# Performance work log

Measured on AMD Instinct MI355X. Metric: run time of the kernel, lower is better.

Reference implementation:

```python
import jax, jax.numpy as jnp
import numpy as np

B, L, D, O = 4, 256, 512, 128

def setup_inputs() -> dict:
    key = jax.random.key(0)
    k1, k2, k3, k4, k5, k6 = jax.random.split(key, 6)
    return {
        "x1": jax.random.normal(k1, (B, L, D), jnp.float32),
        "x2": jax.random.normal(k2, (B, L, D), jnp.float32),
        "bw": jax.random.uniform(k3, (2,), jnp.float32),
        "W_bil": jax.random.normal(k4, (O, D + 1, D + 1), jnp.float32) * 0.02,
        "W_lin": jax.random.normal(k5, (2 * D, O), jnp.float32) * 0.02,
        "b_lin": jax.random.normal(k6, (O,), jnp.float32) * 0.02,
    }

def reference(x1, x2, bw, W_bil, W_lin, b_lin):
    bwn = jax.nn.softmax(bw)
    d1 = x1.shape[-1]
    # Bilinear with bias_x/bias_y: append ones column to x1 and x2.
    ones1 = jnp.ones((*x1.shape[:2], 1), x1.dtype)
    ones2 = jnp.ones((*x2.shape[:2], 1), x2.dtype)
    x1b = jnp.concatenate([x1, ones1], axis=-1)  # [B, L1, D+1]
    x2b = jnp.concatenate([x2, ones2], axis=-1)  # [B, L2, D+1]
    # einsum 'bxi,oij,byj->boxy' then permute(0,2,3,1) -> bxyo
    bilinear_logits = jnp.einsum('bxi,oij,byj->bxyo', x1b, W_bil, x2b)
    # linear over concat([x1 expanded, x2 expanded]) == split-weight broadcast sum
    lin1 = x1 @ W_lin[:d1]   # [B, L1, O]
    lin2 = x2 @ W_lin[d1:]   # [B, L2, O]
    linear_logits = lin1[:, :, None, :] + lin2[:, None, :, :] + b_lin  # [B, L1, L2, O]
    return bwn[0] * bilinear_logits + bwn[1] * linear_logits
```

## Files before the change

kernel.cpp:

```cpp
#include <hip/hip_runtime.h>


#define LL 256
#define DD 512
#define OO 128
#define BB 4
#define WB_OI 263169
#define WB_R512 262656

typedef __attribute__((ext_vector_type(8))) short  short8;
typedef __attribute__((ext_vector_type(8))) unsigned short us8;
typedef __attribute__((ext_vector_type(4))) unsigned short us4;
typedef __attribute__((ext_vector_type(4))) float  f32x4;

__device__ __forceinline__ unsigned short f2bf(float f) {
    unsigned int u = __builtin_bit_cast(unsigned int, f);
    u = (u + 0x7FFFu + ((u >> 16) & 1u)) >> 16;
    return (unsigned short)u;
}
__device__ __forceinline__ float bf2f(unsigned short s) {
    return __builtin_bit_cast(float, (unsigned int)s << 16);
}
__device__ __forceinline__ void load_lds16(const void* g, void* l) {
    __builtin_amdgcn_global_load_lds(
        (const __attribute__((address_space(1))) unsigned int*)g,
        (__attribute__((address_space(3))) unsigned int*)l, 16, 0, 0);
}

__global__ __launch_bounds__(256) void cast2_kernel(
    const float* __restrict__ x1, const float* __restrict__ x2,
    unsigned short* __restrict__ x1b, unsigned short* __restrict__ x2b)
{
    int i = blockIdx.x * 256 + threadIdx.x;
    const float* s; unsigned short* d; int j;
    if (i < 131072) { s = x1; d = x1b; j = i; }
    else            { s = x2; d = x2b; j = i - 131072; }
    float4 v = ((const float4*)s)[j];
    us4 u; u.x = f2bf(v.x); u.y = f2bf(v.y); u.z = f2bf(v.z); u.w = f2bf(v.w);
    *(us4*)(d + (size_t)j * 4) = u;
}

__global__ __launch_bounds__(256) void prepw_kernel(
    const float* __restrict__ Wb, const float* __restrict__ bw,
    unsigned short* __restrict__ Wb16)
{
    const int t = threadIdx.x;
    const int row = blockIdx.x * 4 + (t >> 6);
    const int o = row >> 9, i = row & 511;
    const int l = t & 63;
    const float e0 = __expf(bw[0]), e1 = __expf(bw[1]);
    const float bwn0 = e0 / (e0 + e1);
    const float* src = Wb + (size_t)o * WB_OI + (size_t)i * 513;
    unsigned short* dst = Wb16 + (size_t)row * 512;
    float v[8];
    #pragma unroll
    for (int e = 0; e < 8; ++e) v[e] = src[e * 64 + l];
    #pragma unroll
    for (int e = 0; e < 8; ++e) dst[e * 64 + l] = f2bf(bwn0 * v[e]);
}

__global__ __launch_bounds__(256) void prep512_kernel(
    const float* __restrict__ Wb, float* __restrict__ W512T)
{
    int idx = blockIdx.x * 256 + threadIdx.x;
    if (idx < 513 * 128) {
        const int o = idx & 127, j = idx >> 7;
        W512T[idx] = Wb[(size_t)o * WB_OI + WB_R512 + j];
    }
}

__global__ __launch_bounds__(128) void u512_kernel(
    const float* __restrict__ x2, const float* __restrict__ W512T,
    const float* __restrict__ W_lin, const float* __restrict__ b_lin,
    const float* __restrict__ bw, float* __restrict__ u512buf)
{
    __shared__ float xs[DD];
    const int by = blockIdx.x;
    const int o  = threadIdx.x;
    const float* xr = x2 + (size_t)by * DD;
    for (int j = o; j < DD; j += 128) xs[j] = xr[j];
    __syncthreads();
    float s1 = W512T[512 * 128 + o];
    float s2 = b_lin[o];
    #pragma unroll 4
    for (int j = 0; j < DD; ++j) {
        s1 += xs[j] * W512T[j * 128 + o];
        s2 += xs[j] * W_lin[(size_t)(DD + j) * OO + o];
    }
    const float e0 = __expf(bw[0]), e1 = __expf(bw[1]);
    const float bwn0 = e0 / (e0 + e1), bwn1 = e1 / (e0 + e1);
    u512buf[(size_t)by * OO + o] = bwn0 * s1 + bwn1 * s2;
}

#define PHASE(S, KS) do {                                                       \
    const unsigned short* As_ = (const unsigned short*)(smem + (S) * 32768);    \
    const unsigned short* Bs_ = As_ + 8192;                                     \
    const int ck = (((KS) * 4 + lk) ^ lx7) * 8;                                 \
    short8 af[4], bfr[4];                                                       \
    _Pragma("unroll")                                                           \
    for (int f = 0; f < 4; ++f) af[f]  = *(const short8*)(As_ + (mrow + f * 16) * 64 + ck); \
    _Pragma("unroll")                                                           \
    for (int f = 0; f < 4; ++f) bfr[f] = *(const short8*)(Bs_ + (ncol + f * 16) * 64 + ck); \
    __builtin_amdgcn_s_setprio(1);                                              \
    _Pragma("unroll")                                                           \
    for (int mt = 0; mt < 4; ++mt)                                              \
        _Pragma("unroll")                                                       \
        for (int nt = 0; nt < 4; ++nt)                                          \
            acc[mt][nt] = __builtin_amdgcn_mfma_f32_16x16x32_bf16(af[mt], bfr[nt], acc[mt][nt], 0, 0, 0); \
    __builtin_amdgcn_s_setprio(0);                                              \
  } while (0)

#define WAIT_BAR(N) do {                                                        \
    asm volatile("s_waitcnt vmcnt(" #N ")" ::: "memory");                       \
    __builtin_amdgcn_s_barrier();                                               \
    asm volatile("" ::: "memory");                                              \
  } while (0)

__global__ __launch_bounds__(256) void passA_kernel(
    const unsigned short* __restrict__ x2b, const unsigned short* __restrict__ Wb16,
    const float* __restrict__ W_bil, const float* __restrict__ W_lin,
    const float* __restrict__ bw, unsigned short* __restrict__ Up)
{
    __shared__ __align__(16) char smem[65536];
    unsigned short* Cs  = (unsigned short*)smem;
    float* corr = (float*)(smem + 17408);

    const int t = threadIdx.x, w = t >> 6, l = t & 63;
    const int id  = blockIdx.x;
    const int lin = (id & 7) * 512 + (id >> 3);
    const int o   = lin >> 5;
    const int ib  = (lin & 3) * 128;
    const int yg  = ((lin >> 2) & 7) * 128;
    const int wy = w & 1, wx = w >> 1;

    f32x4 acc[4][4] = {};
    const unsigned short* Wo16 = Wb16 + (size_t)o * DD * DD;

    const int rloc = t >> 3;
    const int csw  = (t & 7) ^ (rloc & 7);

#define STAGE_A(S, KT) do {                                                     \
    unsigned short* As_ = (unsigned short*)(smem + (S) * 32768);                \
    unsigned short* Bs_ = As_ + 8192;                                           \
    const int gc = (KT) * 64 + csw * 8;                                         \
    _Pragma("unroll")                                                           \
    for (int q = 0; q < 4; ++q) {                                               \
        const int row = q * 32 + rloc;                                          \
        load_lds16(x2b  + (size_t)(yg + row) * DD + gc, As_ + q * 2048 + t * 8);\
        load_lds16(Wo16 + (size_t)(ib + row) * DD + gc, Bs_ + q * 2048 + t * 8);\
    } } while (0)

    const int mrow = wy * 64 + (l & 15);
    const int ncol = wx * 64 + (l & 15);
    const int lk   = l >> 4;
    const int lx7  = l & 7;

    STAGE_A(0, 0);
    WAIT_BAR(0);
    #pragma unroll
    for (int kt = 0; kt < 8; ++kt) {
        const int cur = kt & 1;
        if (kt < 7) STAGE_A(cur ^ 1, kt + 1);
        PHASE(cur, 0);
        PHASE(cur, 1);
        WAIT_BAR(0);
    }
#undef STAGE_A

    const float e0 = __expf(bw[0]), e1 = __expf(bw[1]);
    const float bwn0 = e0 / (e0 + e1), bwn1 = e1 / (e0 + e1);
    if (t < 128) {
        const int ig = ib + t;
        corr[t] = bwn1 * W_lin[(size_t)ig * OO + o]
                + bwn0 * W_bil[(size_t)o * WB_OI + (size_t)ig * 513 + 512];
    }
    #pragma unroll
    for (int half = 0; half < 2; ++half) {
        if (wy == half) {
            #pragma unroll
            for (int mt = 0; mt < 4; ++mt) {
                const int yl = mt * 16 + ((l >> 4) << 2);
                #pragma unroll
                for (int nt = 0; nt < 4; ++nt) {
                    const int ic = wx * 64 + nt * 16 + (l & 15);
                    #pragma unroll
                    for (int r = 0; r < 4; ++r)
                        Cs[(yl + r) * 136 + ic] = f2bf(acc[mt][nt][r]);
                }
            }
        }
        __syncthreads();
        #pragma unroll
        for (int p = 0; p < 4; ++p) {
            const int yl = p * 16 + (t >> 4);
            const int i0 = (t & 15) * 8;
            short8 v = *(const short8*)(Cs + yl * 136 + i0);
            us8 uo;
            #pragma unroll
            for (int e = 0; e < 8; ++e)
                uo[e] = f2bf(bf2f((unsigned short)v[e]) + corr[i0 + e]);
            *(us8*)(Up + ((size_t)(yg + half * 64 + yl) * OO + o) * DD + ib + i0) = uo;
        }
        __syncthreads();
    }
}

__global__ __launch_bounds__(256) void passB_kernel(
    const unsigned short* __restrict__ x1b, const unsigned short* __restrict__ Up,
    const float* __restrict__ u512buf, float* __restrict__ out)
{
    __shared__ __align__(16) char smem[65536];

    const int t = threadIdx.x, w = t >> 6, l = t & 63;
    const int xb = blockIdx.x * 128;
    const int yg = blockIdx.y;
    const int bb = yg >> 8, y = yg & 255;
    const int wy = w & 1, wx = w >> 1;

    f32x4 acc[4][4] = {};

    const int rloc = t >> 3;
    const int csw  = (t & 7) ^ (rloc & 7);

#define STAGE_B(S, KT) do {                                                          \
    unsigned short* As_ = (unsigned short*)(smem + (S) * 32768);                     \
    unsigned short* Bs_ = As_ + 8192;                                                \
    const int gc = (KT) * 64 + csw * 8;                                              \
    _Pragma("unroll")                                                                \
    for (int q = 0; q < 4; ++q) {                                                    \
        const int row = q * 32 + rloc;                                               \
        load_lds16(x1b + (size_t)(bb * LL + xb + row) * DD + gc, As_ + q * 2048 + t * 8); \
        load_lds16(Up  + (size_t)(yg * OO + row) * DD + gc,      Bs_ + q * 2048 + t * 8); \
    } } while (0)

    const int mrow = wy * 64 + (l & 15);
    const int ncol = wx * 64 + (l & 15);
    const int lk   = l >> 4;
    const int lx7  = l & 7;

    STAGE_B(0, 0);
    WAIT_BAR(0);
    #pragma unroll
    for (int kt = 0; kt < 8; ++kt) {
        const int cur = kt & 1;
        if (kt < 7) STAGE_B(cur ^ 1, kt + 1);
        PHASE(cur, 0);
        PHASE(cur, 1);
        WAIT_BAR(0);
    }
#undef STAGE_B

    #pragma unroll
    for (int mt = 0; mt < 4; ++mt) {
        const int xr = wy * 64 + mt * 16 + ((l >> 4) << 2);
        #pragma unroll
        for (int nt = 0; nt < 4; ++nt) {
            const int oc = wx * 64 + nt * 16 + (l & 15);
            const float c = u512buf[(size_t)yg * OO + oc];
            #pragma unroll
            for (int r = 0; r < 4; ++r)
                out[((size_t)(bb * LL + xb + xr + r) * LL + y) * OO + oc] = acc[mt][nt][r] + c;
        }
    }
}

extern "C" void kernel_launch(void* const* d_in, const int* in_sizes, int n_in,
                              void* d_out, int out_size, void* d_ws, size_t ws_size,
                              hipStream_t stream)
{
    const float* x1    = (const float*)d_in[0];
    const float* x2    = (const float*)d_in[1];
    const float* bw    = (const float*)d_in[2];
    const float* W_bil = (const float*)d_in[3];
    const float* W_lin = (const float*)d_in[4];
    const float* b_lin = (const float*)d_in[5];
    float* out = (float*)d_out;

    char* ws = (char*)d_ws;
    unsigned short* x1b16 = (unsigned short*)ws;
    unsigned short* x2b16 = (unsigned short*)(ws + (1u << 20));
    float*          u512b = (float*)(ws + (2u << 20));
    float*          W512T = (float*)(ws + (2u << 20) + (512u << 10));
    unsigned short* Wb16  = (unsigned short*)(ws + (3u << 20));
    unsigned short* Up    = (unsigned short*)(ws + (3u << 20) + ((size_t)128 * 512 * 512 * 2));

    cast2_kernel<<<1024, 256, 0, stream>>>(x1, x2, x1b16, x2b16);
    prepw_kernel<<<16384, 256, 0, stream>>>(W_bil, bw, Wb16);
    prep512_kernel<<<257, 256, 0, stream>>>(W_bil, W512T);
    u512_kernel<<<BB * LL, 128, 0, stream>>>(x2, W512T, W_lin, b_lin, bw, u512b);

    passA_kernel<<<4096, 256, 0, stream>>>(x2b16, Wb16, W_bil, W_lin, bw, Up);
    passB_kernel<<<dim3(2, BB * LL), 256, 0, stream>>>(x1b16, Up, u512b, out);
}
```

Before: 484.8 us.

## Load A operand directly to registers, halve LDS, raise occupancy to 3

Both GEMM kernels now fetch the A tile (x1b/x2b rows) straight from global memory into register banks (double-buffered af0/af1) instead of staging it through LDS. Only the B tile stays in LDS, which halves shared memory per block and lets launch bounds request 3 blocks per CU. The explicit vmcnt waits are replaced by __syncthreads. The cost is higher register pressure and less coalesced direct global loads for A, and correctness of the LDS async loads now depends on the barriers alone.

```diff
diff --git a/kernel.cpp b/kernel.cpp
--- a/kernel.cpp
+++ b/kernel.cpp
@@ -92,38 +92,61 @@
     u512buf[(size_t)by * OO + o] = bwn0 * s1 + bwn1 * s2;
 }
 
-#define PHASE(S, KS) do {                                                       \
-    const unsigned short* As_ = (const unsigned short*)(smem + (S) * 32768);    \
-    const unsigned short* Bs_ = As_ + 8192;                                     \
-    const int ck = (((KS) * 4 + lk) ^ lx7) * 8;                                 \
-    short8 af[4], bfr[4];                                                       \
-    _Pragma("unroll")                                                           \
-    for (int f = 0; f < 4; ++f) af[f]  = *(const short8*)(As_ + (mrow + f * 16) * 64 + ck); \
-    _Pragma("unroll")                                                           \
-    for (int f = 0; f < 4; ++f) bfr[f] = *(const short8*)(Bs_ + (ncol + f * 16) * 64 + ck); \
+#define LOADA(BANK, KT) do {                                                    \
+    _Pragma("unroll")                                                           \
+    for (int q = 0; q < 8; ++q) {                                               \
+        const int mt_ = q & 3, ks_ = q >> 2;                                    \
+        BANK[q] = *(const short8*)(Abase + (size_t)(mrow + mt_ * 16) * DD       \
+                                   + (KT) * 64 + ks_ * 32 + kg);                \
+    } } while (0)
+
+#define STAGEB(S, KT) do {                                                      \
+    unsigned short* Bs_ = (unsigned short*)(smem + (S) * 16384);                \
+    const int gc = (KT) * 64 + csw * 8;                                         \
+    _Pragma("unroll")                                                           \
+    for (int q = 0; q < 4; ++q)                                                 \
+        load_lds16(Bbase + (size_t)(q * 32 + (t >> 3)) * DD + gc,               \
+                   Bs_ + q * 2048 + t * 8);                                     \
+    } while (0)
+
+#define CPHASE(S, KS, BANK) do {                                                \
+    const unsigned short* Bs_ = (const unsigned short*)(smem + (S) * 16384);    \
+    short8 bfr[4];                                                              \
+    _Pragma("unroll")                                                           \
+    for (int nt = 0; nt < 4; ++nt)                                              \
+        bfr[nt] = *(const short8*)(Bs_ + (ncol + nt * 16) * 64                  \
+                                   + (((KS) * 4 + lk) ^ lx7) * 8);              \
     __builtin_amdgcn_s_setprio(1);                                              \
     _Pragma("unroll")                                                           \
     for (int mt = 0; mt < 4; ++mt)                                              \
         _Pragma("unroll")                                                       \
         for (int nt = 0; nt < 4; ++nt)                                          \
-            acc[mt][nt] = __builtin_amdgcn_mfma_f32_16x16x32_bf16(af[mt], bfr[nt], acc[mt][nt], 0, 0, 0); \
+            acc[mt][nt] = __builtin_amdgcn_mfma_f32_16x16x32_bf16(              \
+                BANK[(KS) * 4 + mt], bfr[nt], acc[mt][nt], 0, 0, 0);            \
     __builtin_amdgcn_s_setprio(0);                                              \
   } while (0)
 
-#define WAIT_BAR(N) do {                                                        \
-    asm volatile("s_waitcnt vmcnt(" #N ")" ::: "memory");                       \
-    __builtin_amdgcn_s_barrier();                                               \
-    asm volatile("" ::: "memory");                                              \
-  } while (0)
-
-__global__ __launch_bounds__(256) void passA_kernel(
+#define KLOOP(STAGEM)                                                           \
+    STAGEM(0, 0); LOADA(af0, 0);                                                \
+    _Pragma("unroll")                                                           \
+    for (int it = 0; it < 4; ++it) {                                            \
+        const int kt0 = it * 2;                                                 \
+        __syncthreads();                           \
+        STAGEM(1, kt0 + 1); LOADA(af1, kt0 + 1);                                \
+        CPHASE(0, 0, af0); CPHASE(0, 1, af0);                                   \
+        __syncthreads();                              \
+        if (kt0 + 2 < 8) { STAGEM(0, kt0 + 2); LOADA(af0, kt0 + 2); }           \
+        CPHASE(1, 0, af1); CPHASE(1, 1, af1);                                   \
+    }
+
+__global__ __launch_bounds__(256, 3) void passA_kernel(
     const unsigned short* __restrict__ x2b, const unsigned short* __restrict__ Wb16,
     const float* __restrict__ W_bil, const float* __restrict__ W_lin,
     const float* __restrict__ bw, unsigned short* __restrict__ Up)
 {
-    __shared__ __align__(16) char smem[65536];
+    __shared__ __align__(16) char smem[33280];
     unsigned short* Cs  = (unsigned short*)smem;
-    float* corr = (float*)(smem + 17408);
+    float* corr = (float*)(smem + 32768);
 
     const int t = threadIdx.x, w = t >> 6, l = t & 63;
     const int id  = blockIdx.x;
@@ -134,39 +157,20 @@
     const int wy = w & 1, wx = w >> 1;
 
     f32x4 acc[4][4] = {};
-    const unsigned short* Wo16 = Wb16 + (size_t)o * DD * DD;
-
-    const int rloc = t >> 3;
-    const int csw  = (t & 7) ^ (rloc & 7);
-
-#define STAGE_A(S, KT) do {                                                     \
-    unsigned short* As_ = (unsigned short*)(smem + (S) * 32768);                \
-    unsigned short* Bs_ = As_ + 8192;                                           \
-    const int gc = (KT) * 64 + csw * 8;                                         \
-    _Pragma("unroll")                                                           \
-    for (int q = 0; q < 4; ++q) {                                               \
-        const int row = q * 32 + rloc;                                          \
-        load_lds16(x2b  + (size_t)(yg + row) * DD + gc, As_ + q * 2048 + t * 8);\
-        load_lds16(Wo16 + (size_t)(ib + row) * DD + gc, Bs_ + q * 2048 + t * 8);\
-    } } while (0)
-
+    const unsigned short* Abase = x2b + (size_t)yg * DD;
+    const unsigned short* Bbase = Wb16 + (size_t)o * DD * DD + (size_t)ib * DD;
+
+    const int csw  = (t & 7) ^ ((t >> 3) & 7);
     const int mrow = wy * 64 + (l & 15);
     const int ncol = wx * 64 + (l & 15);
+    const int kg   = (l >> 4) * 8;
     const int lk   = l >> 4;
     const int lx7  = l & 7;
 
-    STAGE_A(0, 0);
-    WAIT_BAR(0);
-    #pragma unroll
-    for (int kt = 0; kt < 8; ++kt) {
-        const int cur = kt & 1;
-        if (kt < 7) STAGE_A(cur ^ 1, kt + 1);
-        PHASE(cur, 0);
-        PHASE(cur, 1);
-        WAIT_BAR(0);
-    }
-#undef STAGE_A
-
+    short8 af0[8], af1[8];
+    KLOOP(STAGEB)
+
+    __syncthreads();
     const float e0 = __expf(bw[0]), e1 = __expf(bw[1]);
     const float bwn0 = e0 / (e0 + e1), bwn1 = e1 / (e0 + e1);
     if (t < 128) {
@@ -205,11 +209,11 @@
     }
 }
 
-__global__ __launch_bounds__(256) void passB_kernel(
+__global__ __launch_bounds__(256, 3) void passB_kernel(
     const unsigned short* __restrict__ x1b, const unsigned short* __restrict__ Up,
     const float* __restrict__ u512buf, float* __restrict__ out)
 {
-    __shared__ __align__(16) char smem[65536];
+    __shared__ __align__(16) char smem[32768];
 
     const int t = threadIdx.x, w = t >> 6, l = t & 63;
     const int xb = blockIdx.x * 128;
@@ -218,37 +222,18 @@
     const int wy = w & 1, wx = w >> 1;
 
     f32x4 acc[4][4] = {};
-
-    const int rloc = t >> 3;
-    const int csw  = (t & 7) ^ (rloc & 7);
-
-#define STAGE_B(S, KT) do {                                                          \
-    unsigned short* As_ = (unsigned short*)(smem + (S) * 32768);                     \
-    unsigned short* Bs_ = As_ + 8192;                                                \
-    const int gc = (KT) * 64 + csw * 8;                                              \
-    _Pragma("unroll")                                                                \
-    for (int q = 0; q < 4; ++q) {                                                    \
-        const int row = q * 32 + rloc;                                               \
-        load_lds16(x1b + (size_t)(bb * LL + xb + row) * DD + gc, As_ + q * 2048 + t * 8); \
-        load_lds16(Up  + (size_t)(yg * OO + row) * DD + gc,      Bs_ + q * 2048 + t * 8); \
-    } } while (0)
-
+    const unsigned short* Abase = x1b + (size_t)(bb * LL + xb) * DD;
+    const unsigned short* Bbase = Up + (size_t)yg * OO * DD;
+
+    const int csw  = (t & 7) ^ ((t >> 3) & 7);
     const int mrow = wy * 64 + (l & 15);
     const int ncol = wx * 64 + (l & 15);
+    const int kg   = (l >> 4) * 8;
     const int lk   = l >> 4;
     const int lx7  = l & 7;
 
-    STAGE_B(0, 0);
-    WAIT_BAR(0);
-    #pragma unroll
-    for (int kt = 0; kt < 8; ++kt) {
-        const int cur = kt & 1;
-        if (kt < 7) STAGE_B(cur ^ 1, kt + 1);
-        PHASE(cur, 0);
-        PHASE(cur, 1);
-        WAIT_BAR(0);
-    }
-#undef STAGE_B
+    short8 af0[8], af1[8];
+    KLOOP(STAGEB)
 
     #pragma unroll
     for (int mt = 0; mt < 4; ++mt) {
```

Measured after the change: 541.6 us. 11.7% more time.
